# Optimization experiments

Hardware: AMD Instinct MI355X
Metric: run time of the kernel (lower is better)

## Reference

```python
import jax, jax.numpy as jnp
import numpy as np

NUM_EXPERTS = 8
HIDDEN = 2048
INTER = 1408
TOKENS = 2048
TOP_K = 2


def setup_inputs() -> dict:
    key = jax.random.key(0)
    k1, k2, k3, k4, k5, k6 = jax.random.split(key, 6)
    hidden_states = jax.random.normal(k1, (TOKENS, HIDDEN), dtype=jnp.float32)
    top_k_index = jax.random.randint(k2, (TOKENS, TOP_K), 0, NUM_EXPERTS)
    top_k_weights = jax.random.uniform(k3, (TOKENS, TOP_K), dtype=jnp.float32)
    top_k_weights = top_k_weights / top_k_weights.sum(-1, keepdims=True)  # router-normalized
    scale = 0.02
    Wg = jax.random.normal(k4, (NUM_EXPERTS, INTER, HIDDEN), dtype=jnp.float32) * scale
    Wu = jax.random.normal(k5, (NUM_EXPERTS, INTER, HIDDEN), dtype=jnp.float32) * scale
    Wd = jax.random.normal(k6, (NUM_EXPERTS, HIDDEN, INTER), dtype=jnp.float32) * scale
    return {
        "hidden_states": hidden_states,
        "top_k_index": top_k_index,
        "top_k_weights": top_k_weights,
        "Wg": Wg,
        "Wu": Wu,
        "Wd": Wd,
    }


def reference(hidden_states, top_k_index, top_k_weights, Wg, Wu, Wd):
    # Combine weight per (token, expert): sum over top-k slots routed to that
    # expert (index_add in the original accumulates duplicate routes identically).
    E = Wg.shape[0]
    cw = (jax.nn.one_hot(top_k_index, E, dtype=hidden_states.dtype)
          * top_k_weights[..., None]).sum(axis=1)            # [T, E]
    # Per-expert SwiGLU MLP computed as grouped GEMMs over all tokens.
    gate = jnp.einsum('th,eih->tei', hidden_states, Wg)       # [T, E, I]
    up = jnp.einsum('th,eih->tei', hidden_states, Wu)         # [T, E, I]
    h = jax.nn.silu(gate) * up                                # [T, E, I]
    out_e = jnp.einsum('tei,ehi->teh', h, Wd)                 # [T, E, H]
    # Weighted combine: tokens not routed to an expert have cw == 0.
    return jnp.einsum('teh,te->th', out_e, cw)                # [T, H]
```

## Files before the change

kernel.cpp:

```cpp
#include <hip/hip_runtime.h>
#include <hip/hip_bf16.h>
#include <stdint.h>

#define TOKENS 2048
#define HIDDEN 2048
#define INTER  1408
#define NEXP   8
#define NPAIR  4096

typedef __attribute__((ext_vector_type(8))) short bf16x8;
typedef __attribute__((ext_vector_type(4))) float f32x4;

static __device__ __forceinline__ unsigned short f2b(float f) {
    union { float f; uint32_t u; } v; v.f = f;
    uint32_t r = (v.u + 0x7FFFu + ((v.u >> 16) & 1u)) >> 16;
    return (unsigned short)r;
}

#define GLDS(SRC, DST) \
    __builtin_amdgcn_global_load_lds( \
        (const __attribute__((address_space(1))) unsigned int*)(SRC), \
        (__attribute__((address_space(3))) unsigned int*)(DST), 16, 0, 0)

__global__ void route_k(const int* __restrict__ idx,
                        int* __restrict__ off, int* __restrict__ tok,
                        int* __restrict__ inv) {
    __shared__ int cnt[NEXP];
    __shared__ int cur[NEXP];
    int tid = threadIdx.x;
    if (tid < NEXP) cnt[tid] = 0;
    __syncthreads();
    for (int i = tid; i < NPAIR; i += 256) atomicAdd(&cnt[idx[i]], 1);
    __syncthreads();
    if (tid == 0) {
        int s = 0;
        for (int e = 0; e < NEXP; ++e) { off[e] = s; cur[e] = s; s += cnt[e]; }
        off[NEXP] = s;
    }
    __syncthreads();
    for (int i = tid; i < NPAIR; i += 256) {
        int e = idx[i];
        int p = atomicAdd(&cur[e], 1);
        tok[p] = i >> 1;
        inv[i] = p;
    }
}

__global__ void conv_k(const float* __restrict__ x, unsigned short* __restrict__ xb, int n) {
    int i = (blockIdx.x * blockDim.x + threadIdx.x) * 4;
    if (i < n) {
        float4 v = *(const float4*)(x + i);
        ushort4 o;
        o.x = f2b(v.x); o.y = f2b(v.y); o.z = f2b(v.z); o.w = f2b(v.w);
        *(ushort4*)(xb + i) = o;
    }
}

__global__ void conv3_k(const float* __restrict__ a, unsigned short* __restrict__ ab,
                        const float* __restrict__ b, unsigned short* __restrict__ bb,
                        const float* __restrict__ c, unsigned short* __restrict__ cb,
                        int n4) {
    int stride = gridDim.x * blockDim.x;
    for (int i = blockIdx.x * blockDim.x + threadIdx.x; i < n4; i += stride) {
        int j = i * 4;
        float4 v = *(const float4*)(a + j);
        ushort4 o;
        o.x = f2b(v.x); o.y = f2b(v.y); o.z = f2b(v.z); o.w = f2b(v.w);
        *(ushort4*)(ab + j) = o;
        v = *(const float4*)(b + j);
        o.x = f2b(v.x); o.y = f2b(v.y); o.z = f2b(v.z); o.w = f2b(v.w);
        *(ushort4*)(bb + j) = o;
        v = *(const float4*)(c + j);
        o.x = f2b(v.x); o.y = f2b(v.y); o.z = f2b(v.z); o.w = f2b(v.w);
        *(ushort4*)(cb + j) = o;
    }
}

__global__ void combine_k(const float* __restrict__ tmp, const int* __restrict__ inv,
                          const float* __restrict__ tw, float* __restrict__ out) {
    int i = blockIdx.x * blockDim.x + threadIdx.x;
    int t = i >> 9;
    int c = (i & 511) * 4;
    int p0 = inv[2 * t], p1 = inv[2 * t + 1];
    float w0 = tw[2 * t], w1 = tw[2 * t + 1];
    float4 x = *(const float4*)(tmp + (size_t)p0 * HIDDEN + c);
    float4 y = *(const float4*)(tmp + (size_t)p1 * HIDDEN + c);
    float4 o;
    o.x = w0 * x.x + w1 * y.x;
    o.y = w0 * x.y + w1 * y.y;
    o.z = w0 * x.z + w1 * y.z;
    o.w = w0 * x.w + w1 * y.w;
    *(float4*)(out + (size_t)t * HIDDEN + c) = o;
}


__global__ __launch_bounds__(256, 4) void gemm1_k(
    const unsigned short* __restrict__ Xb,
    const unsigned short* __restrict__ Wgb, const unsigned short* __restrict__ Wub,
    const int* __restrict__ off, const int* __restrict__ tok,
    unsigned short* __restrict__ H) {

    const int e    = blockIdx.x;
    const int o0   = off[e];
    const int cnt  = off[e + 1] - o0;
    const int row0 = blockIdx.y * 128;
    if (row0 >= cnt) return;
    const int col0 = blockIdx.z * 64;

    __shared__ __align__(16) unsigned short sA[2][128 * 32];
    __shared__ __align__(16) unsigned short sG[2][64 * 32];
    __shared__ __align__(16) unsigned short sU[2][64 * 32];
    __shared__ int stok[128];

    const int tid = threadIdx.x;
    if (tid < 128) {
        int r = row0 + tid;
        stok[tid] = tok[o0 + (r < cnt ? r : cnt - 1)];
    }
    __syncthreads();

    int sa_[2]; const unsigned short* gA[2];
    #pragma unroll
    for (int j = 0; j < 2; ++j) {
        int s = tid + 256 * j, r = s >> 2, q = s & 3;
        sa_[j] = s * 8;
        gA[j] = Xb + (size_t)stok[r] * HIDDEN + ((q ^ ((r >> 1) & 3)) << 3);
    }
    int sb_; const unsigned short* gG; const unsigned short* gU;
    {
        int s = tid, r = s >> 2, q = s & 3;
        sb_ = s * 8;
        int c = (q ^ ((r >> 1) & 3)) << 3;
        gG = Wgb + ((size_t)e * INTER + col0 + r) * HIDDEN + c;
        gU = Wub + ((size_t)e * INTER + col0 + r) * HIDDEN + c;
    }

    const int wave = tid >> 6, lane = tid & 63;
    const int wm = (wave >> 1) * 64, wn = (wave & 1) * 32;
    const int lm = lane & 15, quad = lane >> 4;
    const int swz = ((quad ^ ((lane >> 1) & 3)) << 3);

    f32x4 accg[4][2], accu[4][2];
    #pragma unroll
    for (int i = 0; i < 4; ++i)
        #pragma unroll
        for (int j = 0; j < 2; ++j) {
            accg[i][j] = (f32x4){0.f, 0.f, 0.f, 0.f};
            accu[i][j] = (f32x4){0.f, 0.f, 0.f, 0.f};
        }

    GLDS(gA[0], &sA[0][sa_[0]]);
    GLDS(gA[1], &sA[0][sa_[1]]);
    GLDS(gG, &sG[0][sb_]);
    GLDS(gU, &sU[0][sb_]);
    __syncthreads();

    const int NS = HIDDEN / 32;
    for (int ks = 0; ks < NS; ++ks) {
        const int b = ks & 1;
        if (ks + 1 < NS) {
            const int ko = (ks + 1) * 32;
            GLDS(gA[0] + ko, &sA[b ^ 1][sa_[0]]);
            GLDS(gA[1] + ko, &sA[b ^ 1][sa_[1]]);
            GLDS(gG + ko, &sG[b ^ 1][sb_]);
            GLDS(gU + ko, &sU[b ^ 1][sb_]);
        }
        bf16x8 af[4], gf[2], uf[2];
        #pragma unroll
        for (int mi = 0; mi < 4; ++mi)
            af[mi] = *(const bf16x8*)&sA[b][(wm + mi * 16 + lm) * 32 + swz];
        #pragma unroll
        for (int ni = 0; ni < 2; ++ni) {
            gf[ni] = *(const bf16x8*)&sG[b][(wn + ni * 16 + lm) * 32 + swz];
            uf[ni] = *(const bf16x8*)&sU[b][(wn + ni * 16 + lm) * 32 + swz];
        }
        #pragma unroll
        for (int mi = 0; mi < 4; ++mi)
            #pragma unroll
            for (int ni = 0; ni < 2; ++ni) {
                accg[mi][ni] = __builtin_amdgcn_mfma_f32_16x16x32_bf16(af[mi], gf[ni], accg[mi][ni], 0, 0, 0);
                accu[mi][ni] = __builtin_amdgcn_mfma_f32_16x16x32_bf16(af[mi], uf[ni], accu[mi][ni], 0, 0, 0);
            }
        __syncthreads();
    }

    #pragma unroll
    for (int mi = 0; mi < 4; ++mi) {
        #pragma unroll
        for (int reg = 0; reg < 4; ++reg) {
            int lr = wm + mi * 16 + quad * 4 + reg;
            int r  = row0 + lr;
            if (r < cnt) {
                size_t hrow = (size_t)(o0 + r) * INTER;
                #pragma unroll
                for (int ni = 0; ni < 2; ++ni) {
                    float g = accg[mi][ni][reg];
                    float u = accu[mi][ni][reg];
                    float h = g / (1.f + __expf(-g)) * u;
                    H[hrow + col0 + wn + ni * 16 + lm] = f2b(h);
                }
            }
        }
    }
}

__global__ __launch_bounds__(256, 4) void gemm2_k(
    const unsigned short* __restrict__ H,
    const unsigned short* __restrict__ Wdb,
    const int* __restrict__ off,
    float* __restrict__ tmp) {

    const int e    = blockIdx.x;
    const int o0   = off[e];
    const int cnt  = off[e + 1] - o0;
    const int row0 = blockIdx.y * 128;
    if (row0 >= cnt) return;
    const int col0 = blockIdx.z * 128;

    __shared__ __align__(16) unsigned short sA[2][128 * 32];
    __shared__ __align__(16) unsigned short sB[2][128 * 32];

    const int tid = threadIdx.x;

    int sa_[2];
    const unsigned short* gA[2]; const unsigned short* gB[2];
    #pragma unroll
    for (int j = 0; j < 2; ++j) {
        int s = tid + 256 * j, r = s >> 2, q = s & 3;
        sa_[j] = s * 8;
        int c = (q ^ ((r >> 1) & 3)) << 3;
        int gr = row0 + r; if (gr >= cnt) gr = cnt - 1;
        gA[j] = H + (size_t)(o0 + gr) * INTER + c;
        gB[j] = Wdb + ((size_t)e * HIDDEN + col0 + r) * INTER + c;
    }

    const int wave = tid >> 6, lane = tid & 63;
    const int wm = (wave >> 1) * 64, wn = (wave & 1) * 64;
    const int lm = lane & 15, quad = lane >> 4;
    const int swz = ((quad ^ ((lane >> 1) & 3)) << 3);

    f32x4 acc[4][4];
    #pragma unroll
    for (int i = 0; i < 4; ++i)
        #pragma unroll
        for (int j = 0; j < 4; ++j) acc[i][j] = (f32x4){0.f, 0.f, 0.f, 0.f};

    #pragma unroll
    for (int j = 0; j < 2; ++j) {
        GLDS(gA[j], &sA[0][sa_[j]]);
        GLDS(gB[j], &sB[0][sa_[j]]);
    }
    __syncthreads();

    const int NS = INTER / 32;
    for (int ks = 0; ks < NS; ++ks) {
        const int b = ks & 1;
        if (ks + 1 < NS) {
            const int ko = (ks + 1) * 32;
            #pragma unroll
            for (int j = 0; j < 2; ++j) {
                GLDS(gA[j] + ko, &sA[b ^ 1][sa_[j]]);
                GLDS(gB[j] + ko, &sB[b ^ 1][sa_[j]]);
            }
        }
        bf16x8 af[4], bf[4];
        #pragma unroll
        for (int mi = 0; mi < 4; ++mi)
            af[mi] = *(const bf16x8*)&sA[b][(wm + mi * 16 + lm) * 32 + swz];
        #pragma unroll
        for (int ni = 0; ni < 4; ++ni)
            bf[ni] = *(const bf16x8*)&sB[b][(wn + ni * 16 + lm) * 32 + swz];
        #pragma unroll
        for (int mi = 0; mi < 4; ++mi)
            #pragma unroll
            for (int ni = 0; ni < 4; ++ni)
                acc[mi][ni] = __builtin_amdgcn_mfma_f32_16x16x32_bf16(af[mi], bf[ni], acc[mi][ni], 0, 0, 0);
        __syncthreads();
    }

    #pragma unroll
    for (int mi = 0; mi < 4; ++mi) {
        #pragma unroll
        for (int reg = 0; reg < 4; ++reg) {
            int lr = wm + mi * 16 + quad * 4 + reg;
            int r  = row0 + lr;
            if (r < cnt) {
                size_t trow = (size_t)(o0 + r) * HIDDEN;
                #pragma unroll
                for (int ni = 0; ni < 4; ++ni)
                    tmp[trow + col0 + wn + ni * 16 + lm] = acc[mi][ni][reg];
            }
        }
    }
}

extern "C" void kernel_launch(void* const* d_in, const int* in_sizes, int n_in,
                              void* d_out, int out_size, void* d_ws, size_t ws_size,
                              hipStream_t stream) {
    const float* X   = (const float*)d_in[0];
    const int*   idx = (const int*)d_in[1];
    const float* tw  = (const float*)d_in[2];
    const float* Wg  = (const float*)d_in[3];
    const float* Wu  = (const float*)d_in[4];
    const float* Wd  = (const float*)d_in[5];
    float* out = (float*)d_out;

    char* ws = (char*)d_ws;
    const size_t OFF_TOK = 64;
    const size_t OFF_INV = OFF_TOK + (size_t)NPAIR * 4;
    const size_t OFF_XB  = 65536;
    const size_t OFF_H   = OFF_XB + (size_t)TOKENS * HIDDEN * 2;
    const size_t WELEMS  = (size_t)NEXP * INTER * HIDDEN;
    const size_t OFF_WG  = OFF_H + (size_t)NPAIR * INTER * 2;
    const size_t OFF_WU  = OFF_WG + WELEMS * 2;
    const size_t OFF_WD  = OFF_WU + WELEMS * 2;
    const size_t OFF_TMP = OFF_WD + WELEMS * 2;

    int*            off = (int*)ws;
    int*            tok = (int*)(ws + OFF_TOK);
    int*            inv = (int*)(ws + OFF_INV);
    unsigned short* Xb  = (unsigned short*)(ws + OFF_XB);
    unsigned short* H   = (unsigned short*)(ws + OFF_H);
    unsigned short* Wgb = (unsigned short*)(ws + OFF_WG);
    unsigned short* Wub = (unsigned short*)(ws + OFF_WU);
    unsigned short* Wdb = (unsigned short*)(ws + OFF_WD);
    float*          tmp = (float*)(ws + OFF_TMP);

    route_k<<<1, 256, 0, stream>>>(idx, off, tok, inv);
    conv_k<<<(TOKENS * HIDDEN / 4 + 255) / 256, 256, 0, stream>>>(X, Xb, TOKENS * HIDDEN);
    conv3_k<<<4096, 256, 0, stream>>>(Wg, Wgb, Wu, Wub, Wd, Wdb, (int)(WELEMS / 4));

    gemm1_k<<<dim3(NEXP, NPAIR / 128, INTER / 64), 256, 0, stream>>>(Xb, Wgb, Wub, off, tok, H);
    gemm2_k<<<dim3(NEXP, NPAIR / 128, HIDDEN / 128), 256, 0, stream>>>(H, Wdb, off, tmp);
    combine_k<<<TOKENS * (HIDDEN / 4) / 256, 256, 0, stream>>>(tmp, inv, tw, out);
}
```

Before: 492.6 us.

## Fuse fp32-to-bf16 weight conversion into GEMM tile loads and reorder grid

```diff
diff --git a/kernel.cpp b/kernel.cpp
--- a/kernel.cpp
+++ b/kernel.cpp
@@ -15,6 +15,12 @@
     union { float f; uint32_t u; } v; v.f = f;
     uint32_t r = (v.u + 0x7FFFu + ((v.u >> 16) & 1u)) >> 16;
     return (unsigned short)r;
+}
+
+static __device__ __forceinline__ uint32_t cvtpk(float lo, float hi) {
+    uint32_t r;
+    asm("v_cvt_pk_bf16_f32 %0, %1, %2" : "=v"(r) : "v"(lo), "v"(hi));
+    return r;
 }
 
 #define GLDS(SRC, DST) \
@@ -53,26 +59,6 @@
         ushort4 o;
         o.x = f2b(v.x); o.y = f2b(v.y); o.z = f2b(v.z); o.w = f2b(v.w);
         *(ushort4*)(xb + i) = o;
-    }
-}
-
-__global__ void conv3_k(const float* __restrict__ a, unsigned short* __restrict__ ab,
-                        const float* __restrict__ b, unsigned short* __restrict__ bb,
-                        const float* __restrict__ c, unsigned short* __restrict__ cb,
-                        int n4) {
-    int stride = gridDim.x * blockDim.x;
-    for (int i = blockIdx.x * blockDim.x + threadIdx.x; i < n4; i += stride) {
-        int j = i * 4;
-        float4 v = *(const float4*)(a + j);
-        ushort4 o;
-        o.x = f2b(v.x); o.y = f2b(v.y); o.z = f2b(v.z); o.w = f2b(v.w);
-        *(ushort4*)(ab + j) = o;
-        v = *(const float4*)(b + j);
-        o.x = f2b(v.x); o.y = f2b(v.y); o.z = f2b(v.z); o.w = f2b(v.w);
-        *(ushort4*)(bb + j) = o;
-        v = *(const float4*)(c + j);
-        o.x = f2b(v.x); o.y = f2b(v.y); o.z = f2b(v.z); o.w = f2b(v.w);
-        *(ushort4*)(cb + j) = o;
     }
 }
 
@@ -96,16 +82,16 @@
 
 __global__ __launch_bounds__(256, 4) void gemm1_k(
     const unsigned short* __restrict__ Xb,
-    const unsigned short* __restrict__ Wgb, const unsigned short* __restrict__ Wub,
+    const float* __restrict__ Wg, const float* __restrict__ Wu,
     const int* __restrict__ off, const int* __restrict__ tok,
     unsigned short* __restrict__ H) {
 
-    const int e    = blockIdx.x;
+    const int e    = blockIdx.z;
     const int o0   = off[e];
     const int cnt  = off[e + 1] - o0;
     const int row0 = blockIdx.y * 128;
     if (row0 >= cnt) return;
-    const int col0 = blockIdx.z * 64;
+    const int col0 = blockIdx.x * 64;
 
     __shared__ __align__(16) unsigned short sA[2][128 * 32];
     __shared__ __align__(16) unsigned short sG[2][64 * 32];
@@ -126,13 +112,13 @@
         sa_[j] = s * 8;
         gA[j] = Xb + (size_t)stok[r] * HIDDEN + ((q ^ ((r >> 1) & 3)) << 3);
     }
-    int sb_; const unsigned short* gG; const unsigned short* gU;
+    int sb_; const float* fG; const float* fU;
     {
         int s = tid, r = s >> 2, q = s & 3;
         sb_ = s * 8;
         int c = (q ^ ((r >> 1) & 3)) << 3;
-        gG = Wgb + ((size_t)e * INTER + col0 + r) * HIDDEN + c;
-        gU = Wub + ((size_t)e * INTER + col0 + r) * HIDDEN + c;
+        fG = Wg + ((size_t)e * INTER + col0 + r) * HIDDEN + c;
+        fU = Wu + ((size_t)e * INTER + col0 + r) * HIDDEN + c;
     }
 
     const int wave = tid >> 6, lane = tid & 63;
@@ -151,19 +137,30 @@
 
     GLDS(gA[0], &sA[0][sa_[0]]);
     GLDS(gA[1], &sA[0][sa_[1]]);
-    GLDS(gG, &sG[0][sb_]);
-    GLDS(gU, &sU[0][sb_]);
+    {
+        float4 g0 = *(const float4*)(fG);
+        float4 g1 = *(const float4*)(fG + 4);
+        float4 u0 = *(const float4*)(fU);
+        float4 u1 = *(const float4*)(fU + 4);
+        *(int4*)&sG[0][sb_] = make_int4(cvtpk(g0.x, g0.y), cvtpk(g0.z, g0.w),
+                                        cvtpk(g1.x, g1.y), cvtpk(g1.z, g1.w));
+        *(int4*)&sU[0][sb_] = make_int4(cvtpk(u0.x, u0.y), cvtpk(u0.z, u0.w),
+                                        cvtpk(u1.x, u1.y), cvtpk(u1.z, u1.w));
+    }
     __syncthreads();
 
     const int NS = HIDDEN / 32;
     for (int ks = 0; ks < NS; ++ks) {
         const int b = ks & 1;
+        float4 g0, g1, u0, u1;
         if (ks + 1 < NS) {
             const int ko = (ks + 1) * 32;
             GLDS(gA[0] + ko, &sA[b ^ 1][sa_[0]]);
             GLDS(gA[1] + ko, &sA[b ^ 1][sa_[1]]);
-            GLDS(gG + ko, &sG[b ^ 1][sb_]);
-            GLDS(gU + ko, &sU[b ^ 1][sb_]);
+            g0 = *(const float4*)(fG + ko);
+            g1 = *(const float4*)(fG + ko + 4);
+            u0 = *(const float4*)(fU + ko);
+            u1 = *(const float4*)(fU + ko + 4);
         }
         bf16x8 af[4], gf[2], uf[2];
         #pragma unroll
@@ -181,6 +178,12 @@
                 accg[mi][ni] = __builtin_amdgcn_mfma_f32_16x16x32_bf16(af[mi], gf[ni], accg[mi][ni], 0, 0, 0);
                 accu[mi][ni] = __builtin_amdgcn_mfma_f32_16x16x32_bf16(af[mi], uf[ni], accu[mi][ni], 0, 0, 0);
             }
+        if (ks + 1 < NS) {
+            *(int4*)&sG[b ^ 1][sb_] = make_int4(cvtpk(g0.x, g0.y), cvtpk(g0.z, g0.w),
+                                                cvtpk(g1.x, g1.y), cvtpk(g1.z, g1.w));
+            *(int4*)&sU[b ^ 1][sb_] = make_int4(cvtpk(u0.x, u0.y), cvtpk(u0.z, u0.w),
+                                                cvtpk(u1.x, u1.y), cvtpk(u1.z, u1.w));
+        }
         __syncthreads();
     }
 
@@ -206,24 +209,23 @@
 
 __global__ __launch_bounds__(256, 4) void gemm2_k(
     const unsigned short* __restrict__ H,
-    const unsigned short* __restrict__ Wdb,
+    const float* __restrict__ Wd,
     const int* __restrict__ off,
     float* __restrict__ tmp) {
 
-    const int e    = blockIdx.x;
+    const int e    = blockIdx.z;
     const int o0   = off[e];
     const int cnt  = off[e + 1] - o0;
     const int row0 = blockIdx.y * 128;
     if (row0 >= cnt) return;
-    const int col0 = blockIdx.z * 128;
+    const int col0 = blockIdx.x * 64;
 
     __shared__ __align__(16) unsigned short sA[2][128 * 32];
-    __shared__ __align__(16) unsigned short sB[2][128 * 32];
+    __shared__ __align__(16) unsigned short sB[2][64 * 32];
 
     const int tid = threadIdx.x;
 
-    int sa_[2];
-    const unsigned short* gA[2]; const unsigned short* gB[2];
+    int sa_[2]; const unsigned short* gA[2];
     #pragma unroll
     for (int j = 0; j < 2; ++j) {
         int s = tid + 256 * j, r = s >> 2, q = s & 3;
@@ -231,50 +233,63 @@
         int c = (q ^ ((r >> 1) & 3)) << 3;
         int gr = row0 + r; if (gr >= cnt) gr = cnt - 1;
         gA[j] = H + (size_t)(o0 + gr) * INTER + c;
-        gB[j] = Wdb + ((size_t)e * HIDDEN + col0 + r) * INTER + c;
+    }
+    int sb_; const float* fB;
+    {
+        int s = tid, r = s >> 2, q = s & 3;
+        sb_ = s * 8;
+        int c = (q ^ ((r >> 1) & 3)) << 3;
+        fB = Wd + ((size_t)e * HIDDEN + col0 + r) * INTER + c;
     }
 
     const int wave = tid >> 6, lane = tid & 63;
-    const int wm = (wave >> 1) * 64, wn = (wave & 1) * 64;
+    const int wm = (wave >> 1) * 64, wn = (wave & 1) * 32;
     const int lm = lane & 15, quad = lane >> 4;
     const int swz = ((quad ^ ((lane >> 1) & 3)) << 3);
 
-    f32x4 acc[4][4];
+    f32x4 acc[4][2];
     #pragma unroll
     for (int i = 0; i < 4; ++i)
         #pragma unroll
-        for (int j = 0; j < 4; ++j) acc[i][j] = (f32x4){0.f, 0.f, 0.f, 0.f};
-
-    #pragma unroll
-    for (int j = 0; j < 2; ++j) {
-        GLDS(gA[j], &sA[0][sa_[j]]);
-        GLDS(gB[j], &sB[0][sa_[j]]);
+        for (int j = 0; j < 2; ++j) acc[i][j] = (f32x4){0.f, 0.f, 0.f, 0.f};
+
+    GLDS(gA[0], &sA[0][sa_[0]]);
+    GLDS(gA[1], &sA[0][sa_[1]]);
+    {
+        float4 b0 = *(const float4*)(fB);
+        float4 b1 = *(const float4*)(fB + 4);
+        *(int4*)&sB[0][sb_] = make_int4(cvtpk(b0.x, b0.y), cvtpk(b0.z, b0.w),
+                                        cvtpk(b1.x, b1.y), cvtpk(b1.z, b1.w));
     }
     __syncthreads();
 
     const int NS = INTER / 32;
     for (int ks = 0; ks < NS; ++ks) {
         const int b = ks & 1;
+        float4 b0, b1;
         if (ks + 1 < NS) {
             const int ko = (ks + 1) * 32;
-            #pragma unroll
-            for (int j = 0; j < 2; ++j) {
-                GLDS(gA[j] + ko, &sA[b ^ 1][sa_[j]]);
-                GLDS(gB[j] + ko, &sB[b ^ 1][sa_[j]]);
-            }
-        }
-        bf16x8 af[4], bf[4];
+            GLDS(gA[0] + ko, &sA[b ^ 1][sa_[0]]);
+            GLDS(gA[1] + ko, &sA[b ^ 1][sa_[1]]);
+            b0 = *(const float4*)(fB + ko);
+            b1 = *(const float4*)(fB + ko + 4);
+        }
+        bf16x8 af[4], bf[2];
         #pragma unroll
         for (int mi = 0; mi < 4; ++mi)
             af[mi] = *(const bf16x8*)&sA[b][(wm + mi * 16 + lm) * 32 + swz];
         #pragma unroll
-        for (int ni = 0; ni < 4; ++ni)
+        for (int ni = 0; ni < 2; ++ni)
             bf[ni] = *(const bf16x8*)&sB[b][(wn + ni * 16 + lm) * 32 + swz];
         #pragma unroll
         for (int mi = 0; mi < 4; ++mi)
             #pragma unroll
-            for (int ni = 0; ni < 4; ++ni)
+            for (int ni = 0; ni < 2; ++ni)
                 acc[mi][ni] = __builtin_amdgcn_mfma_f32_16x16x32_bf16(af[mi], bf[ni], acc[mi][ni], 0, 0, 0);
+        if (ks + 1 < NS) {
+            *(int4*)&sB[b ^ 1][sb_] = make_int4(cvtpk(b0.x, b0.y), cvtpk(b0.z, b0.w),
+                                                cvtpk(b1.x, b1.y), cvtpk(b1.z, b1.w));
+        }
         __syncthreads();
     }
 
@@ -287,7 +302,7 @@
             if (r < cnt) {
                 size_t trow = (size_t)(o0 + r) * HIDDEN;
                 #pragma unroll
-                for (int ni = 0; ni < 4; ++ni)
+                for (int ni = 0; ni < 2; ++ni)
                     tmp[trow + col0 + wn + ni * 16 + lm] = acc[mi][ni][reg];
             }
         }
@@ -310,27 +325,19 @@
     const size_t OFF_INV = OFF_TOK + (size_t)NPAIR * 4;
     const size_t OFF_XB  = 65536;
     const size_t OFF_H   = OFF_XB + (size_t)TOKENS * HIDDEN * 2;
-    const size_t WELEMS  = (size_t)NEXP * INTER * HIDDEN;
-    const size_t OFF_WG  = OFF_H + (size_t)NPAIR * INTER * 2;
-    const size_t OFF_WU  = OFF_WG + WELEMS * 2;
-    const size_t OFF_WD  = OFF_WU + WELEMS * 2;
-    const size_t OFF_TMP = OFF_WD + WELEMS * 2;
+    const size_t OFF_TMP = OFF_H + (size_t)NPAIR * INTER * 2;
 
     int*            off = (int*)ws;
     int*            tok = (int*)(ws + OFF_TOK);
     int*            inv = (int*)(ws + OFF_INV);
     unsigned short* Xb  = (unsigned short*)(ws + OFF_XB);
     unsigned short* H   = (unsigned short*)(ws + OFF_H);
-    unsigned short* Wgb = (unsigned short*)(ws + OFF_WG);
-    unsigned short* Wub = (unsigned short*)(ws + OFF_WU);
-    unsigned short* Wdb = (unsigned short*)(ws + OFF_WD);
     float*          tmp = (float*)(ws + OFF_TMP);
 
     route_k<<<1, 256, 0, stream>>>(idx, off, tok, inv);
     conv_k<<<(TOKENS * HIDDEN / 4 + 255) / 256, 256, 0, stream>>>(X, Xb, TOKENS * HIDDEN);
-    conv3_k<<<4096, 256, 0, stream>>>(Wg, Wgb, Wu, Wub, Wd, Wdb, (int)(WELEMS / 4));
-
-    gemm1_k<<<dim3(NEXP, NPAIR / 128, INTER / 64), 256, 0, stream>>>(Xb, Wgb, Wub, off, tok, H);
-    gemm2_k<<<dim3(NEXP, NPAIR / 128, HIDDEN / 128), 256, 0, stream>>>(H, Wdb, off, tmp);
+
+    gemm1_k<<<dim3(INTER / 64, NPAIR / 128, NEXP), 256, 0, stream>>>(Xb, Wg, Wu, off, tok, H);
+    gemm2_k<<<dim3(HIDDEN / 64, NPAIR / 128, NEXP), 256, 0, stream>>>(H, Wd, off, tmp);
     combine_k<<<TOKENS * (HIDDEN / 4) / 256, 256, 0, stream>>>(tmp, inv, tw, out);
 }
```

After: 433.8 us. 1.14x faster.
